# Optimization experiments

Hardware: AMD Instinct MI355X
Metric: run time of the kernel (lower is better)

## Reference

```python
import jax, jax.numpy as jnp
import numpy as np

B, N, K = 8, 4096, 16
N_STEPS = 4
DT = 0.05
EPS = 1e-8


def symmetrize(M):
    return 0.5 * (M + jnp.swapaxes(M, -1, -2))


def ensure_spd(S, eps):
    # Project to SPD cone via eigenvalue clipping: V max(L, eps) V^T
    Kd = S.shape[-1]
    S = symmetrize(S + eps * jnp.eye(Kd, dtype=S.dtype))
    w, U = jnp.linalg.eigh(S)
    w = jnp.clip(w, eps, None)
    return symmetrize((U * w[..., None, :]) @ jnp.swapaxes(U, -1, -2))


def spd_exponential_map(Sigma, V, eps=EPS):
    # exp_Sigma(V) = S^{1/2} exp(S^{-1/2} V S^{-1/2}) S^{1/2}
    Kd = Sigma.shape[-1]
    Sigma = symmetrize(Sigma) + eps * jnp.eye(Kd, dtype=Sigma.dtype)
    w, U = jnp.linalg.eigh(Sigma)
    w = jnp.clip(w, eps, None)
    sq = jnp.sqrt(w)
    Ut = jnp.swapaxes(U, -1, -2)
    S_sqrt = (U * sq[..., None, :]) @ Ut
    S_isqrt = (U * (1.0 / sq)[..., None, :]) @ Ut
    W = symmetrize(S_isqrt @ V @ S_isqrt)
    ww, Uw = jnp.linalg.eigh(W)
    ww = jnp.clip(ww, -20.0, 20.0)
    expW = (Uw * jnp.exp(ww)[..., None, :]) @ jnp.swapaxes(Uw, -1, -2)
    return ensure_spd(S_sqrt @ expW @ S_sqrt, eps)


def spd_kinetic_gradient(Sigma, pi_Sigma):
    # dT/dSigma = 2 pi Sigma pi, symmetrized
    return symmetrize(2.0 * (pi_Sigma @ Sigma) @ pi_Sigma)


def retract_to_principal_ball(phi, margin=0.01):
    eps = 1e-12
    r_max = jnp.pi - margin
    theta = jnp.linalg.norm(phi, axis=-1, keepdims=True)
    theta_safe = jnp.maximum(theta, eps)
    axis = phi / theta_safe
    two_pi = 2.0 * jnp.pi
    tw = jnp.remainder(theta, two_pi)
    flip = tw > jnp.pi
    tf = jnp.where(flip, two_pi - tw, tw)
    af = jnp.where(flip, -axis, axis)
    tf = jnp.minimum(tf, r_max)
    return af * tf


def setup_inputs() -> dict:
    key = jax.random.key(0)
    ks = jax.random.split(key, 7)
    mu = jax.random.normal(ks[0], (B, N, K), dtype=jnp.float32)
    A = 0.3 * jax.random.normal(ks[1], (B, N, K, K), dtype=jnp.float32)
    Sigma = A @ jnp.swapaxes(A, -1, -2) + jnp.eye(K, dtype=jnp.float32)
    phi = 0.5 * jax.random.normal(ks[2], (B, N, 3), dtype=jnp.float32)
    pi_mu = 0.1 * jax.random.normal(ks[3], (B, N, K), dtype=jnp.float32)
    pi_Sigma = symmetrize(0.05 * jax.random.normal(ks[4], (B, N, K, K), dtype=jnp.float32))
    pi_phi = 0.1 * jax.random.normal(ks[5], (B, N, 3), dtype=jnp.float32)
    Bm = 0.3 * jax.random.normal(ks[6], (B, N, K, K), dtype=jnp.float32)
    M_inv = Bm @ jnp.swapaxes(Bm, -1, -2) + jnp.eye(K, dtype=jnp.float32)
    return {"mu": mu, "Sigma": Sigma, "phi": phi,
            "pi_mu": pi_mu, "pi_Sigma": pi_Sigma, "pi_phi": pi_phi,
            "M_inv": M_inv}


def reference(mu, Sigma, phi, pi_mu, pi_Sigma, pi_phi, M_inv):
    dt = DT
    for _ in range(N_STEPS):  # fixed small leapfrog step count
        # half-step momentum kick from curved-geometry kinetic force
        pi_Sigma = symmetrize(pi_Sigma - 0.5 * dt * spd_kinetic_gradient(Sigma, pi_Sigma))
        # full-step position drift
        mu = mu + dt * jnp.einsum('bnij,bnj->bni', M_inv, pi_mu)
        Sigma_dot = 2.0 * Sigma @ pi_Sigma @ Sigma  # dSigma/dt from Legendre transform
        Sigma = spd_exponential_map(Sigma, dt * Sigma_dot, EPS)
        phi = retract_to_principal_ball(phi + dt * pi_phi)
        # second half-step momentum kick
        pi_Sigma = symmetrize(pi_Sigma - 0.5 * dt * spd_kinetic_gradient(Sigma, pi_Sigma))
    return (mu, Sigma, phi)
```

## Files before the change

### kernel.cpp

```cpp
#include <hip/hip_runtime.h>
#include <math.h>

typedef float f32x4 __attribute__((ext_vector_type(4)));
typedef _Float16 f16x4 __attribute__((ext_vector_type(4)));

#define MFMA_F16 __builtin_amdgcn_mfma_f32_16x16x16f16

namespace {
constexpr float DT = 0.05f;
constexpr int NSTEPS = 4;

struct Split { f16x4 h; f16x4 l; };

__device__ __forceinline__ f16x4 mkh(f32x4 v) {
  f16x4 h;
#pragma unroll
  for (int i = 0; i < 4; ++i) h[i] = (_Float16)v[i];
  return h;
}

__device__ __forceinline__ Split mksplit(f32x4 v) {
  Split s;
#pragma unroll
  for (int i = 0; i < 4; ++i) s.h[i] = (_Float16)v[i];
#pragma unroll
  for (int i = 0; i < 4; ++i)
    s.l[i] = (_Float16)fmaf(-1.0f, (float)s.h[i], v[i]);
  return s;
}

__device__ __forceinline__ f32x4 mm3(Split a, Split b) {
  f32x4 acc = {0.f, 0.f, 0.f, 0.f};
  acc = MFMA_F16(a.h, b.h, acc, 0, 0, 0);
  acc = MFMA_F16(a.h, b.l, acc, 0, 0, 0);
  acc = MFMA_F16(a.l, b.h, acc, 0, 0, 0);
  return acc;
}
__device__ __forceinline__ f32x4 mm2(Split a, f16x4 bh) {
  f32x4 acc = {0.f, 0.f, 0.f, 0.f};
  acc = MFMA_F16(a.h, bh, acc, 0, 0, 0);
  acc = MFMA_F16(a.l, bh, acc, 0, 0, 0);
  return acc;
}
__device__ __forceinline__ f32x4 mm1(f16x4 ah, f16x4 bh) {
  f32x4 acc = {0.f, 0.f, 0.f, 0.f};
  acc = MFMA_F16(ah, bh, acc, 0, 0, 0);
  return acc;
}
}

__global__ __launch_bounds__(256) void ham_leapfrog(
    const float* __restrict__ mu, const float* __restrict__ Sigma,
    const float* __restrict__ phi, const float* __restrict__ pi_mu,
    const float* __restrict__ pi_Sigma, const float* __restrict__ pi_phi,
    const float* __restrict__ M_inv, float* __restrict__ out, int n_elem) {
  const int wave = threadIdx.x >> 6;
  const int lane = threadIdx.x & 63;
  const int e = blockIdx.x * (blockDim.x >> 6) + wave;
  if (e >= n_elem) return;

  const int c = lane & 15;
  const int r0 = (lane >> 4) * 4;
  const size_t eb = (size_t)e * 256;

  f32x4 Sg, Dv, Mi;
#pragma unroll
  for (int j = 0; j < 4; ++j) {
    Sg[j] = Sigma[eb + (size_t)(r0 + j) * 16 + c];
    Dv[j] = pi_Sigma[eb + (size_t)(r0 + j) * 16 + c];
    Mi[j] = M_inv[eb + (size_t)(r0 + j) * 16 + c];
  }
  Dv = (2.0f * DT) * Dv;

  const float pmc = pi_mu[(size_t)e * 16 + c];
  f32x4 am = Mi * pmc;
#pragma unroll
  for (int m = 1; m < 16; m <<= 1) {
#pragma unroll
    for (int j = 0; j < 4; ++j) am[j] += __shfl_xor(am[j], m);
  }

  float p0 = phi[(size_t)e * 3 + 0];
  float p1 = phi[(size_t)e * 3 + 1];
  float p2 = phi[(size_t)e * 3 + 2];
  const float q0 = DT * pi_phi[(size_t)e * 3 + 0];
  const float q1 = DT * pi_phi[(size_t)e * 3 + 1];
  const float q2 = DT * pi_phi[(size_t)e * 3 + 2];
  const float TWO_PI = 6.28318530717958647692f;
  const float INV_2PI = 0.15915494309189533577f;
  const float PI_F = 3.14159265358979323846f;
  const float R_MAX = 3.13159265358979323846f;
#pragma unroll
  for (int s = 0; s < NSTEPS; ++s) {
    p0 += q0; p1 += q1; p2 += q2;
    float th = sqrtf(p0 * p0 + p1 * p1 + p2 * p2);
    float inv = 1.0f / fmaxf(th, 1e-12f);
    float tw = th - TWO_PI * floorf(th * INV_2PI);
    bool flip = tw > PI_F;
    float tf = flip ? (TWO_PI - tw) : tw;
    float sgn = flip ? -1.f : 1.f;
    tf = fminf(tf, R_MAX);
    float f = sgn * inv * tf;
    p0 *= f; p1 *= f; p2 *= f;
  }

  Split sS = mksplit(Sg);
  Split sD = mksplit(Dv);

  for (int step = 0; step < NSTEPS; ++step) {
    {
      f32x4 T = mm3(sS, sD);
      Split sT = mksplit(T);
      f32x4 K = mm3(sD, sT);
      Dv = Dv - 0.5f * K;
      sD = mksplit(Dv);
    }
    {
      f32x4 ACC = Sg;
      f32x4 U = mm3(sD, sS);
      Split sU = mksplit(U);
      f32x4 Y = mm3(sS, sU);
      ACC += Y;
      f16x4 yh = mkh(Y);
      U = mm2(sD, yh);
      f16x4 uh = mkh(U);
      Y = mm2(sS, uh);
      ACC += 0.5f * Y;
      yh = mkh(Y);
      U = mm1(sD.h, yh); uh = mkh(U);
      Y = mm1(sS.h, uh); ACC += (1.0f / 6.0f) * Y; yh = mkh(Y);
      U = mm1(sD.h, yh); uh = mkh(U);
      Y = mm1(sS.h, uh); ACC += (1.0f / 24.0f) * Y; yh = mkh(Y);
      U = mm1(sD.h, yh); uh = mkh(U);
      Y = mm1(sS.h, uh); ACC += (1.0f / 120.0f) * Y;
      Sg = ACC;
      sS = mksplit(Sg);
    }
    {
      f32x4 T = mm3(sS, sD);
      Split sT = mksplit(T);
      f32x4 K = mm3(sD, sT);
      Dv = Dv - 0.5f * K;
      sD = mksplit(Dv);
    }
  }

  float* out_mu = out;
  float* out_Sg = out + (size_t)n_elem * 16;
  float* out_ph = out + (size_t)n_elem * (16 + 256);

#pragma unroll
  for (int j = 0; j < 4; ++j)
    out_Sg[eb + (size_t)(r0 + j) * 16 + c] = Sg[j];

  if (c == 0) {
#pragma unroll
    for (int j = 0; j < 4; ++j)
      out_mu[(size_t)e * 16 + r0 + j] =
          mu[(size_t)e * 16 + r0 + j] + ((float)NSTEPS * DT) * am[j];
  }
  if (lane == 0) {
    out_ph[(size_t)e * 3 + 0] = p0;
    out_ph[(size_t)e * 3 + 1] = p1;
    out_ph[(size_t)e * 3 + 2] = p2;
  }
}

extern "C" void kernel_launch(void* const* d_in, const int* in_sizes, int n_in,
                              void* d_out, int out_size, void* d_ws, size_t ws_size,
                              hipStream_t stream) {
  const float* mu       = (const float*)d_in[0];
  const float* Sigma    = (const float*)d_in[1];
  const float* phi      = (const float*)d_in[2];
  const float* pi_mu    = (const float*)d_in[3];
  const float* pi_Sigma = (const float*)d_in[4];
  const float* pi_phi   = (const float*)d_in[5];
  const float* M_inv    = (const float*)d_in[6];
  float* o = (float*)d_out;

  const int n_elem = in_sizes[0] / 16;
  const int waves_per_block = 4;
  const int blocks = (n_elem + waves_per_block - 1) / waves_per_block;
  hipLaunchKernelGGL(ham_leapfrog, dim3(blocks), dim3(256), 0, stream,
                     mu, Sigma, phi, pi_mu, pi_Sigma, pi_phi, M_inv, o, n_elem);
}
```

Baseline: 184.8 us.

## Refactor SPD exponential series to reuse one product and cut MFMA/convert counts

Restructures the Taylor series for the Sigma update so that X = D*S is formed once and each higher term is Z*X, which halves the matmuls per term. It also reduces the kinetic gradient products from three-pass split precision to two-pass, and uses packed round-toward-zero conversions for fp16 splitting. The M_inv*pi_mu reduction moves from shuffle reductions to a single MFMA in fp16, and 32-bit indexing, rcp and full loop unrolling are added. These changes trade fp32 accuracy for fewer MFMA and conversion instructions. The fp16 mu path and RTZ rounding may raise error.

```diff
diff --git a/kernel.cpp b/kernel.cpp
--- a/kernel.cpp
+++ b/kernel.cpp
@@ -3,6 +3,8 @@
 
 typedef float f32x4 __attribute__((ext_vector_type(4)));
 typedef _Float16 f16x4 __attribute__((ext_vector_type(4)));
+typedef __fp16 fp16x2 __attribute__((ext_vector_type(2)));
+typedef __fp16 fp16x4 __attribute__((ext_vector_type(4)));
 
 #define MFMA_F16 __builtin_amdgcn_mfma_f32_16x16x16f16
 
@@ -12,20 +14,20 @@
 
 struct Split { f16x4 h; f16x4 l; };
 
-__device__ __forceinline__ f16x4 mkh(f32x4 v) {
-  f16x4 h;
-#pragma unroll
-  for (int i = 0; i < 4; ++i) h[i] = (_Float16)v[i];
-  return h;
+__device__ __forceinline__ f16x4 pk4(f32x4 v) {
+  fp16x2 a = __builtin_amdgcn_cvt_pkrtz(v[0], v[1]);
+  fp16x2 b = __builtin_amdgcn_cvt_pkrtz(v[2], v[3]);
+  fp16x4 r = __builtin_shufflevector(a, b, 0, 1, 2, 3);
+  return __builtin_bit_cast(f16x4, r);
 }
 
 __device__ __forceinline__ Split mksplit(f32x4 v) {
   Split s;
+  s.h = pk4(v);
+  f32x4 hf;
 #pragma unroll
-  for (int i = 0; i < 4; ++i) s.h[i] = (_Float16)v[i];
-#pragma unroll
-  for (int i = 0; i < 4; ++i)
-    s.l[i] = (_Float16)fmaf(-1.0f, (float)s.h[i], v[i]);
+  for (int i = 0; i < 4; ++i) hf[i] = (float)s.h[i];
+  s.l = pk4(v - hf);
   return s;
 }
 
@@ -61,31 +63,30 @@
 
   const int c = lane & 15;
   const int r0 = (lane >> 4) * 4;
-  const size_t eb = (size_t)e * 256;
+  const int eb = e * 256;
+  const int ev = e * 16;
 
   f32x4 Sg, Dv, Mi;
 #pragma unroll
   for (int j = 0; j < 4; ++j) {
-    Sg[j] = Sigma[eb + (size_t)(r0 + j) * 16 + c];
-    Dv[j] = pi_Sigma[eb + (size_t)(r0 + j) * 16 + c];
-    Mi[j] = M_inv[eb + (size_t)(r0 + j) * 16 + c];
+    const int off = eb + (r0 + j) * 16 + c;
+    Sg[j] = Sigma[off];
+    Dv[j] = pi_Sigma[off];
+    Mi[j] = M_inv[off];
   }
   Dv = (2.0f * DT) * Dv;
 
-  const float pmc = pi_mu[(size_t)e * 16 + c];
-  f32x4 am = Mi * pmc;
-#pragma unroll
-  for (int m = 1; m < 16; m <<= 1) {
-#pragma unroll
-    for (int j = 0; j < 4; ++j) am[j] += __shfl_xor(am[j], m);
-  }
+  f32x4 pm4 = *(const f32x4*)(pi_mu + ev + r0);
+  f16x4 Ph = pk4(pm4);
+  if (c != 0) Ph = (f16x4)(_Float16)0;
+  f32x4 am = mm1(pk4(Mi), Ph);
 
-  float p0 = phi[(size_t)e * 3 + 0];
-  float p1 = phi[(size_t)e * 3 + 1];
-  float p2 = phi[(size_t)e * 3 + 2];
-  const float q0 = DT * pi_phi[(size_t)e * 3 + 0];
-  const float q1 = DT * pi_phi[(size_t)e * 3 + 1];
-  const float q2 = DT * pi_phi[(size_t)e * 3 + 2];
+  float p0 = phi[e * 3 + 0];
+  float p1 = phi[e * 3 + 1];
+  float p2 = phi[e * 3 + 2];
+  const float q0 = DT * pi_phi[e * 3 + 0];
+  const float q1 = DT * pi_phi[e * 3 + 1];
+  const float q2 = DT * pi_phi[e * 3 + 2];
   const float TWO_PI = 6.28318530717958647692f;
   const float INV_2PI = 0.15915494309189533577f;
   const float PI_F = 3.14159265358979323846f;
@@ -94,7 +95,7 @@
   for (int s = 0; s < NSTEPS; ++s) {
     p0 += q0; p1 += q1; p2 += q2;
     float th = sqrtf(p0 * p0 + p1 * p1 + p2 * p2);
-    float inv = 1.0f / fmaxf(th, 1e-12f);
+    float inv = __builtin_amdgcn_rcpf(fmaxf(th, 1e-12f));
     float tw = th - TWO_PI * floorf(th * INV_2PI);
     bool flip = tw > PI_F;
     float tf = flip ? (TWO_PI - tw) : tw;
@@ -107,39 +108,30 @@
   Split sS = mksplit(Sg);
   Split sD = mksplit(Dv);
 
+#pragma unroll
   for (int step = 0; step < NSTEPS; ++step) {
     {
       f32x4 T = mm3(sS, sD);
-      Split sT = mksplit(T);
-      f32x4 K = mm3(sD, sT);
+      f32x4 K = mm2(sD, pk4(T));
       Dv = Dv - 0.5f * K;
       sD = mksplit(Dv);
     }
     {
-      f32x4 ACC = Sg;
-      f32x4 U = mm3(sD, sS);
-      Split sU = mksplit(U);
-      f32x4 Y = mm3(sS, sU);
-      ACC += Y;
-      f16x4 yh = mkh(Y);
-      U = mm2(sD, yh);
-      f16x4 uh = mkh(U);
-      Y = mm2(sS, uh);
-      ACC += 0.5f * Y;
-      yh = mkh(Y);
-      U = mm1(sD.h, yh); uh = mkh(U);
-      Y = mm1(sS.h, uh); ACC += (1.0f / 6.0f) * Y; yh = mkh(Y);
-      U = mm1(sD.h, yh); uh = mkh(U);
-      Y = mm1(sS.h, uh); ACC += (1.0f / 24.0f) * Y; yh = mkh(Y);
-      U = mm1(sD.h, yh); uh = mkh(U);
-      Y = mm1(sS.h, uh); ACC += (1.0f / 120.0f) * Y;
+      f32x4 X = mm3(sD, sS);
+      Split sX = mksplit(X);
+      f32x4 Z = mm3(sS, sX);
+      f32x4 ACC = Sg + Z;
+      f16x4 zh = pk4(Z);
+      Z = mm1(zh, sX.h); ACC += (1.0f / 2.0f) * Z; zh = pk4(Z);
+      Z = mm1(zh, sX.h); ACC += (1.0f / 6.0f) * Z; zh = pk4(Z);
+      Z = mm1(zh, sX.h); ACC += (1.0f / 24.0f) * Z; zh = pk4(Z);
+      Z = mm1(zh, sX.h); ACC += (1.0f / 120.0f) * Z;
       Sg = ACC;
       sS = mksplit(Sg);
     }
     {
       f32x4 T = mm3(sS, sD);
-      Split sT = mksplit(T);
-      f32x4 K = mm3(sD, sT);
+      f32x4 K = mm2(sD, pk4(T));
       Dv = Dv - 0.5f * K;
       sD = mksplit(Dv);
     }
@@ -151,18 +143,16 @@
 
 #pragma unroll
   for (int j = 0; j < 4; ++j)
-    out_Sg[eb + (size_t)(r0 + j) * 16 + c] = Sg[j];
+    out_Sg[eb + (r0 + j) * 16 + c] = Sg[j];
 
   if (c == 0) {
-#pragma unroll
-    for (int j = 0; j < 4; ++j)
-      out_mu[(size_t)e * 16 + r0 + j] =
-          mu[(size_t)e * 16 + r0 + j] + ((float)NSTEPS * DT) * am[j];
+    f32x4 mu4 = *(const f32x4*)(mu + ev + r0);
+    *(f32x4*)(out_mu + ev + r0) = mu4 + ((float)NSTEPS * DT) * am;
   }
   if (lane == 0) {
-    out_ph[(size_t)e * 3 + 0] = p0;
-    out_ph[(size_t)e * 3 + 1] = p1;
-    out_ph[(size_t)e * 3 + 2] = p2;
+    out_ph[e * 3 + 0] = p0;
+    out_ph[e * 3 + 1] = p1;
+    out_ph[e * 3 + 2] = p2;
   }
 }
 
```

Result: faster. 163.6 us (-11.5%).
